# Optimization experiments

Hardware: AMD Instinct MI355X
Metric: run time of the kernel (lower is better)

The kernel has to match this reference:

```python
import jax, jax.numpy as jnp
import numpy as np

B, N, CIN, H, D, K = 8, 1000, 16, 64, 16, 3  # batch, nodes, in_dim, hidden, embed_dim, cheb_k
XIN = CIN + H  # GRU concat input dim


def setup_inputs() -> dict:
    key = jax.random.key(0)
    ks = jax.random.split(key, 18)
    f = lambda k, s, sc=1.0: jax.random.normal(k, s, dtype=jnp.float32) * sc
    inp = {}
    inp['x1'] = f(ks[0], (B, N, CIN)); inp['x2'] = f(ks[1], (B, N, CIN)); inp['x3'] = f(ks[2], (B, N, CIN))
    inp['state1'] = f(ks[3], (B, N, H)); inp['state2'] = f(ks[4], (B, N, H)); inp['state3'] = f(ks[5], (B, N, H))
    for i, name in enumerate(['support1', 'support2', 'support3']):
        a = jax.random.uniform(ks[6 + i], (N, N), dtype=jnp.float32)
        inp[name] = a / a.sum(-1, keepdims=True)  # row-stochastic graph, keeps Chebyshev stable
    inp['embeddings1'] = f(ks[9], (N, D), 0.1); inp['embeddings2'] = f(ks[10], (N, D), 0.1); inp['embeddings3'] = f(ks[11], (N, D), 0.1)
    inp['mode_embedding'] = f(ks[12], (3, D), 0.5)
    # xavier-normal-ish scales for the hypernet weight pools
    inp['Wg'] = f(ks[13], (D, K * XIN, 2 * H), (2.0 / (K * XIN * 2 * H + D * 2 * H)) ** 0.5)
    inp['Bg'] = f(ks[14], (D, 2 * H), (2.0 / (D + 2 * H)) ** 0.5)
    inp['Wu'] = f(ks[15], (D, K * XIN, H), (2.0 / (K * XIN * H + D * H)) ** 0.5)
    inp['Bu'] = f(ks[16], (D, H), (2.0 / (D + H)) ** 0.5)
    return inp


def _cheb_gcn(x, support, emb, wp, bp):
    # x:[B,N,C], support:[N,N], emb:[N,D], wp:[D,K*C,O], bp:[D,O]
    # Chebyshev recurrence applied directly to features (equivalent to building T_k(support))
    terms = [x, jnp.einsum('nm,bmc->bnc', support, x)]
    for _ in range(2, K):
        terms.append(2.0 * jnp.einsum('nm,bmc->bnc', support, terms[-1]) - terms[-2])
    x_g = jnp.concatenate(terms, axis=-1)  # [B,N,K*C]
    # meta_axis='S': per-node weights = emb @ wp ; fused contraction
    out = jnp.einsum('bni,nd,dio->bno', x_g, emb, wp) + emb @ bp  # [B,N,O]
    return out


def _cell(x, state, support, emb, me, Wg, Bg, Wu, Bu):
    # me:[D] mode embedding scales the shared pools (einsum 'mc,cdf->mcdf' -> pick mode m)
    zr = jax.nn.sigmoid(_cheb_gcn(jnp.concatenate([x, state], -1), support, emb,
                                  me[:, None, None] * Wg, me[:, None] * Bg))
    z, r = jnp.split(zr, 2, axis=-1)
    hc = jnp.tanh(_cheb_gcn(jnp.concatenate([x, z * state], -1), support, emb,
                            me[:, None, None] * Wu, me[:, None] * Bu))
    return r * state + (1.0 - r) * hc


def reference(x1, x2, x3, state1, state2, state3, support1, support2, support3,
              embeddings1, embeddings2, embeddings3, mode_embedding, Wg, Bg, Wu, Bu):
    h1 = _cell(x1, state1, support1, embeddings1, mode_embedding[0], Wg, Bg, Wu, Bu)
    h2 = _cell(x2, state2, support2, embeddings2, mode_embedding[1], Wg, Bg, Wu, Bu)
    h3 = _cell(x3, state3, support3, embeddings3, mode_embedding[2], Wg, Bg, Wu, Bu)
    return (h1, h2, h3)
```

## Files before the change

### kernel.cpp

```cpp
#include <hip/hip_runtime.h>
#include <math.h>


typedef __attribute__((ext_vector_type(8))) short s16x8;
typedef __attribute__((ext_vector_type(4))) float f32x4;
typedef unsigned short u16;
typedef unsigned int u32;
typedef unsigned long long u64;

__device__ __forceinline__ u32 f2bf(float f) {
  union { float f; u32 u; } v; v.f = f;
  return (v.u + 0x7FFFu + ((v.u >> 16) & 1u)) >> 16;
}
__device__ __forceinline__ float bf2f(u16 h) {
  union { u32 u; float f; } v; v.u = (u32)h << 16; return v.f;
}
__device__ __forceinline__ void glds16(const u16* g, u16* l) {
  __builtin_amdgcn_global_load_lds(
      (const __attribute__((address_space(1))) void*)g,
      (__attribute__((address_space(3))) void*)l, 16, 0, 0);
}

#define E0 3145728
#define E1 1966080
#define E2 1920000
#define E3 384000
#define E4 384000
#define E5 384000
#define E6 119808

struct PrepArgs {
  const float* x[3]; const float* st[3]; const float* S[3];
  u16 *S16, *Xt, *Ag, *AgU, *T1t, *ZSt, *SZ1t;
};

__global__ void prep(PrepArgs P) {
  long idx = (long)blockIdx.x * 256 + threadIdx.x;
  if (idx < E0) {
    int m = (int)(idx >> 20); int rem = (int)(idx & 1048575);
    int n = rem >> 10, k = rem & 1023;
    float v = (n < 1000 && k < 1000) ? P.S[m][n * 1000 + k] : 0.f;
    P.S16[(size_t)m * 1048576 + rem] = (u16)f2bf(v); return;
  }
  idx -= E0;
  if (idx < E1) {
    int m = (int)(idx / 655360); int rem = (int)(idx % 655360);
    int col = rem >> 10, nn = rem & 1023;
    int b = col / 80, c = col % 80;
    float v = 0.f;
    if (nn < 1000) v = (c < 16) ? P.x[m][(b * 1000 + nn) * 16 + c]
                                : P.st[m][(b * 1000 + nn) * 64 + c - 16];
    P.Xt[(size_t)m * 655360 + rem] = (u16)f2bf(v); return;
  }
  idx -= E1;
  if (idx < E2) {
    int m = (int)(idx / 640000); int rem = (int)(idx % 640000);
    int r = rem / 80, c = rem % 80;
    int n = r >> 3, b = r & 7;
    float v = (c < 16) ? P.x[m][(b * 1000 + n) * 16 + c]
                       : P.st[m][(b * 1000 + n) * 64 + c - 16];
    P.Ag[(size_t)m * 2048000 + (size_t)r * 256 + c] = (u16)f2bf(v); return;
  }
  idx -= E2;
  if (idx < E3) {
    int m = (int)(idx / 128000); int rem = (int)(idx % 128000);
    int r = rem / 16, c = 240 + rem % 16;
    P.Ag[(size_t)m * 2048000 + (size_t)r * 256 + c] = 0; return;
  }
  idx -= E3;
  if (idx < E4) {
    int m = (int)(idx / 128000); int rem = (int)(idx % 128000);
    int r = rem / 16, c = rem % 16;
    int n = r >> 3, b = r & 7;
    P.AgU[(size_t)m * 2048000 + (size_t)r * 256 + c] =
        (u16)f2bf(P.x[m][(b * 1000 + n) * 16 + c]); return;
  }
  idx -= E4;
  if (idx < E5) {
    int m = (int)(idx / 128000); int rem = (int)(idx % 128000);
    int r = rem / 16, c = 240 + rem % 16;
    P.AgU[(size_t)m * 2048000 + (size_t)r * 256 + c] = 0; return;
  }
  idx -= E5;
  if (idx < E6) {
    int m = (int)(idx / 39936); int rem = (int)(idx % 39936);
    if (rem < 15360) { int col = rem / 24, j = rem % 24;
      P.T1t[(size_t)m * 655360 + col * 1024 + 1000 + j] = 0; }
    else if (rem < 27648) { int e = rem - 15360; int col = e / 24, j = e % 24;
      P.ZSt[(size_t)m * 524288 + col * 1024 + 1000 + j] = 0; }
    else { int e = rem - 27648; int col = e / 24, j = e % 24;
      P.SZ1t[(size_t)m * 524288 + col * 1024 + 1000 + j] = 0; }
    return;
  }
}

__global__ void bias_kernel(const float* __restrict__ e0, const float* __restrict__ e1,
                            const float* __restrict__ e2, const float* __restrict__ me,
                            const float* __restrict__ Bp, int O, float* __restrict__ outB) {
  int idx = blockIdx.x * blockDim.x + threadIdx.x;
  int total = 3 * 1000 * O;
  if (idx >= total) return;
  int mode = idx / (1000 * O);
  int rem  = idx % (1000 * O);
  int n = rem / O, o = rem % O;
  const float* emb = (mode == 0) ? e0 : (mode == 1) ? e1 : e2;
  float s = 0.f;
#pragma unroll
  for (int d = 0; d < 16; ++d)
    s += emb[n * 16 + d] * me[mode * 16 + d] * Bp[d * O + o];
  outB[idx] = s;
}

__global__ void packW_kernel(const float* __restrict__ Wg, const float* __restrict__ Wu,
                             u16* __restrict__ BtG, u16* __restrict__ BtU) {
  int idx = blockIdx.x * blockDim.x + threadIdx.x;
  if (idx >= (2048 + 1024) * 256) return;
  if (idx < 2048 * 256) {
    int col = idx >> 8, k = idx & 255;
    int d = col >> 7, o = col & 127;
    BtG[idx] = (k < 240) ? (u16)f2bf(Wg[d * 30720 + k * 128 + o]) : (u16)0;
  } else {
    int i2 = idx - 2048 * 256;
    int col = i2 >> 8, k = i2 & 255;
    int d = col >> 6, o = col & 63;
    BtU[i2] = (k < 240) ? (u16)f2bf(Wu[d * 15360 + k * 64 + o]) : (u16)0;
  }
}

struct ChebArgs2 {
  const u16* S16[3]; const u16* A[3]; const u16* Res[3];
  u16* Yt[3]; u16* AgA[3]; u16* AgX[3];
};

__global__ __launch_bounds__(256, 2) void cheb_v4(ChebArgs2 g, int fdiv, int agbase,
                                                  float alpha, float beta, int flags) {
  const int mode = blockIdx.z;
  const u16* __restrict__ Ab = g.A[mode];
  const u16* __restrict__ Sb = g.S16[mode];

  __shared__ u16 As[64 * 64];
  __shared__ u16 Bs[64 * 64];

  const int t = threadIdx.x;
  const int row0 = blockIdx.y * 64, n0 = blockIdx.x * 64;
  const int lane = t & 63, wid = t >> 6;
  const int l16 = lane & 15, quad = lane >> 4;
  const int wy = (wid >> 1) * 32, wx = (wid & 1) * 32;

  f32x4 acc[2][2];
#pragma unroll
  for (int a = 0; a < 2; ++a)
#pragma unroll
    for (int b = 0; b < 2; ++b) acc[a][b] = (f32x4){0.f, 0.f, 0.f, 0.f};

  for (int k0 = 0; k0 < 1024; k0 += 64) {
#pragma unroll
    for (int p = 0; p < 2; ++p) {
      int idx = p * 256 + t; int row = idx >> 3; int cs = (idx & 7) ^ (row & 7);
      glds16(Ab + (size_t)(row0 + row) * 1024 + k0 + cs * 8, &As[idx * 8]);
    }
#pragma unroll
    for (int p = 0; p < 2; ++p) {
      int idx = p * 256 + t; int row = idx >> 3; int cs = (idx & 7) ^ (row & 7);
      glds16(Sb + (size_t)(n0 + row) * 1024 + k0 + cs * 8, &Bs[idx * 8]);
    }
    __syncthreads();
    s16x8 af[2][2], bf[2][2];
#pragma unroll
    for (int mi = 0; mi < 2; ++mi) {
      int row = wy + mi * 16 + l16;
#pragma unroll
      for (int ks = 0; ks < 2; ++ks) {
        int cl = (ks * 4 + quad) ^ (row & 7);
        af[mi][ks] = *(const s16x8*)&As[row * 64 + cl * 8];
      }
    }
#pragma unroll
    for (int ni = 0; ni < 2; ++ni) {
      int row = wx + ni * 16 + l16;
#pragma unroll
      for (int ks = 0; ks < 2; ++ks) {
        int cl = (ks * 4 + quad) ^ (row & 7);
        bf[ni][ks] = *(const s16x8*)&Bs[row * 64 + cl * 8];
      }
    }
#pragma unroll
    for (int ks = 0; ks < 2; ++ks)
#pragma unroll
      for (int mi = 0; mi < 2; ++mi)
#pragma unroll
        for (int ni = 0; ni < 2; ++ni)
          acc[mi][ni] = __builtin_amdgcn_mfma_f32_16x16x32_bf16(af[mi][ks], bf[ni][ks], acc[mi][ni], 0, 0, 0);
    __syncthreads();
  }

#pragma unroll
  for (int mi = 0; mi < 2; ++mi) {
    int frow0 = row0 + wy + mi * 16 + quad * 4;
    int b = frow0 / fdiv, c0 = frow0 - b * fdiv;
#pragma unroll
    for (int ni = 0; ni < 2; ++ni) {
      int n = n0 + wx + ni * 16 + l16;
      if (n < 1000) {
        u16 pk[4];
#pragma unroll
        for (int r = 0; r < 4; ++r) {
          float v = alpha * acc[mi][ni][r];
          if (flags & 1) v += beta * bf2f(g.Res[mode][(size_t)(frow0 + r) * 1024 + n]);
          u16 h = (u16)f2bf(v);
          pk[r] = h;
          if (flags & 2) g.Yt[mode][(size_t)(frow0 + r) * 1024 + n] = h;
        }
        u64 pv = (u64)pk[0] | ((u64)pk[1] << 16) | ((u64)pk[2] << 32) | ((u64)pk[3] << 48);
        *(u64*)&g.AgA[mode][(size_t)(n * 8 + b) * 256 + agbase + c0] = pv;
        if ((flags & 4) && c0 < 16)
          *(u64*)&g.AgX[mode][(size_t)(n * 8 + b) * 256 + agbase + c0] = pv;
      }
    }
  }
}

struct Meta3Args {
  const u16* Ag;
  const u16* Bt;
  const float* emb[3];
  const float* me;
  const float* Bias;
  const float* state[3];
  u16* ZSt;
  u16* AgU;
  float* Rb;
  float* out;
};

__global__ __launch_bounds__(256, 2) void meta3(Meta3Args A, int is_gate, int O) {
  const int mode = blockIdx.z;
  const int row0 = blockIdx.y * 64;
  const int n0 = row0 >> 3;

  __shared__ u16 As[64 * 256];
  __shared__ u16 Bs[64 * 256];
  __shared__ float ewS[8][17];

  const int t = threadIdx.x;
  if (t < 128) {
    int nl = t >> 4, d = t & 15;
    ewS[nl][d] = A.emb[mode][(n0 + nl) * 16 + d] * A.me[mode * 16 + d];
  }

  const int lane = t & 63, wid = t >> 6;
  const int l16 = lane & 15, quad = lane >> 4;
  const int wy = (wid >> 1) * 32, wx = (wid & 1) * 32;
  const u16* Agm = A.Ag + (size_t)mode * 2048000;

#pragma unroll
  for (int p = 0; p < 8; ++p) {
    int idx = p * 256 + t; int row = idx >> 5; int cs = (idx & 31) ^ (row & 7);
    glds16(Agm + (size_t)(row0 + row) * 256 + cs * 8, &As[idx * 8]);
  }
  __syncthreads();

  s16x8 afr[2][8];
#pragma unroll
  for (int mi = 0; mi < 2; ++mi) {
    int row = wy + mi * 16 + l16;
#pragma unroll
    for (int ki = 0; ki < 8; ++ki) {
      int cl = (ki * 4 + quad) ^ (row & 7);
      afr[mi][ki] = *(const s16x8*)&As[row * 256 + cl * 8];
    }
  }

  f32x4 outacc[2][2][2];
#pragma unroll
  for (int a = 0; a < 2; ++a)
#pragma unroll
    for (int b = 0; b < 2; ++b)
#pragma unroll
      for (int c = 0; c < 2; ++c) outacc[a][b][c] = (f32x4){0.f, 0.f, 0.f, 0.f};

  const int shift = (O == 128) ? 1 : 0;
  const int ntiles = O >> 2;

  for (int tl = 0; tl < ntiles; ++tl) {
    const int d = tl >> shift;
    const int oc = tl & shift;
    __syncthreads();
    const int brow0 = d * O + oc * 64;
#pragma unroll
    for (int p = 0; p < 8; ++p) {
      int idx = p * 256 + t; int row = idx >> 5; int cs = (idx & 31) ^ (row & 7);
      glds16(A.Bt + (size_t)(brow0 + row) * 256 + cs * 8, &Bs[idx * 8]);
    }
    __syncthreads();

    f32x4 acc[2][2];
#pragma unroll
    for (int a = 0; a < 2; ++a)
#pragma unroll
      for (int b = 0; b < 2; ++b) acc[a][b] = (f32x4){0.f, 0.f, 0.f, 0.f};

#pragma unroll
    for (int ki = 0; ki < 8; ++ki) {
      s16x8 bfr[2];
#pragma unroll
      for (int ni = 0; ni < 2; ++ni) {
        int row = wx + ni * 16 + l16;
        int cl = (ki * 4 + quad) ^ (row & 7);
        bfr[ni] = *(const s16x8*)&Bs[row * 256 + cl * 8];
      }
#pragma unroll
      for (int mi = 0; mi < 2; ++mi)
#pragma unroll
        for (int ni = 0; ni < 2; ++ni)
          acc[mi][ni] = __builtin_amdgcn_mfma_f32_16x16x32_bf16(afr[mi][ki], bfr[ni], acc[mi][ni], 0, 0, 0);
    }

#pragma unroll
    for (int mi = 0; mi < 2; ++mi) {
      int nl = (wy + mi * 16 + quad * 4) >> 3;
      float s = ewS[nl][d];
#pragma unroll
      for (int ni = 0; ni < 2; ++ni)
#pragma unroll
        for (int r = 0; r < 4; ++r)
          outacc[oc][mi][ni][r] += s * acc[mi][ni][r];
    }
  }

#pragma unroll
  for (int oc = 0; oc <= shift; ++oc)
#pragma unroll
    for (int mi = 0; mi < 2; ++mi)
#pragma unroll
      for (int ni = 0; ni < 2; ++ni)
#pragma unroll
        for (int r = 0; r < 4; ++r) {
          int row = row0 + wy + mi * 16 + quad * 4 + r;
          int n = row >> 3, b = row & 7;
          int o = oc * 64 + wx + ni * 16 + l16;
          float pre = outacc[oc][mi][ni][r] + A.Bias[(size_t)mode * 1000 * O + n * O + o];
          if (is_gate) {
            float sg = 1.f / (1.f + __expf(-pre));
            if (o < 64) {
              float st = A.state[mode][(b * 1000 + n) * 64 + o];
              float zs = sg * st;
              A.ZSt[(size_t)mode * 524288 + (size_t)(b * 64 + o) * 1024 + n] = (u16)f2bf(zs);
              A.AgU[(size_t)mode * 2048000 + (size_t)row * 256 + 16 + o] = (u16)f2bf(zs);
            } else {
              A.Rb[(size_t)mode * 512000 + row * 64 + (o - 64)] = sg;
            }
          } else {
            float hc = tanhf(pre);
            float rr = A.Rb[(size_t)mode * 512000 + row * 64 + o];
            float st = A.state[mode][(b * 1000 + n) * 64 + o];
            A.out[(size_t)mode * 512000 + (b * 1000 + n) * 64 + o] = rr * st + (1.f - rr) * hc;
          }
        }
}

extern "C" void kernel_launch(void* const* d_in, const int* in_sizes, int n_in,
                              void* d_out, int out_size, void* d_ws, size_t ws_size,
                              hipStream_t stream) {
  const float* x[3]   = {(const float*)d_in[0], (const float*)d_in[1], (const float*)d_in[2]};
  const float* st[3]  = {(const float*)d_in[3], (const float*)d_in[4], (const float*)d_in[5]};
  const float* S[3]   = {(const float*)d_in[6], (const float*)d_in[7], (const float*)d_in[8]};
  const float* emb[3] = {(const float*)d_in[9], (const float*)d_in[10], (const float*)d_in[11]};
  const float* me = (const float*)d_in[12];
  const float* Wg = (const float*)d_in[13];
  const float* Bg = (const float*)d_in[14];
  const float* Wu = (const float*)d_in[15];
  const float* Bu = (const float*)d_in[16];
  float* out = (float*)d_out;

  float* BiG = (float*)d_ws;
  float* BiU = BiG + 384000;
  float* Rb  = BiU + 192000;
  u16* S16 = (u16*)(Rb + 1536000);
  u16* Xt  = S16 + 3145728;
  u16* T1t = Xt + 1966080;
  u16* ZSt = T1t + 1966080;
  u16* SZ1t= ZSt + 1572864;
  u16* Ag  = SZ1t + 1572864;
  u16* AgU = Ag + 6144000;
  u16* BtG = AgU + 6144000;
  u16* BtU = BtG + 524288;

  {
    PrepArgs P;
    for (int m = 0; m < 3; ++m) { P.x[m] = x[m]; P.st[m] = st[m]; P.S[m] = S[m]; }
    P.S16 = S16; P.Xt = Xt; P.Ag = Ag; P.AgU = AgU; P.T1t = T1t; P.ZSt = ZSt; P.SZ1t = SZ1t;
    prep<<<32436, 256, 0, stream>>>(P);
  }
  bias_kernel<<<1500, 256, 0, stream>>>(emb[0], emb[1], emb[2], me, Bg, 128, BiG);
  bias_kernel<<<750, 256, 0, stream>>>(emb[0], emb[1], emb[2], me, Bu, 64, BiU);
  packW_kernel<<<3072, 256, 0, stream>>>(Wg, Wu, BtG, BtU);

  {
    ChebArgs2 a;
    for (int m = 0; m < 3; ++m) {
      a.S16[m] = S16 + (size_t)m * 1048576; a.A[m] = Xt + (size_t)m * 655360;
      a.Res[m] = nullptr; a.Yt[m] = T1t + (size_t)m * 655360;
      a.AgA[m] = Ag + (size_t)m * 2048000; a.AgX[m] = AgU + (size_t)m * 2048000;
    }
    cheb_v4<<<dim3(16, 10, 3), 256, 0, stream>>>(a, 80, 80, 1.f, 0.f, 2 | 4);
  }
  {
    ChebArgs2 a;
    for (int m = 0; m < 3; ++m) {
      a.S16[m] = S16 + (size_t)m * 1048576; a.A[m] = T1t + (size_t)m * 655360;
      a.Res[m] = Xt + (size_t)m * 655360; a.Yt[m] = nullptr;
      a.AgA[m] = Ag + (size_t)m * 2048000; a.AgX[m] = AgU + (size_t)m * 2048000;
    }
    cheb_v4<<<dim3(16, 10, 3), 256, 0, stream>>>(a, 80, 160, 2.f, -1.f, 1 | 4);
  }
  {
    Meta3Args a;
    a.Ag = Ag; a.Bt = BtG; a.me = me; a.Bias = BiG;
    a.ZSt = ZSt; a.AgU = AgU; a.Rb = Rb; a.out = out;
    for (int m = 0; m < 3; ++m) { a.emb[m] = emb[m]; a.state[m] = st[m]; }
    meta3<<<dim3(1, 125, 3), 256, 0, stream>>>(a, 1, 128);
  }
  {
    ChebArgs2 a;
    for (int m = 0; m < 3; ++m) {
      a.S16[m] = S16 + (size_t)m * 1048576; a.A[m] = ZSt + (size_t)m * 524288;
      a.Res[m] = nullptr; a.Yt[m] = SZ1t + (size_t)m * 524288;
      a.AgA[m] = AgU + (size_t)m * 2048000; a.AgX[m] = nullptr;
    }
    cheb_v4<<<dim3(16, 8, 3), 256, 0, stream>>>(a, 64, 96, 1.f, 0.f, 2);
  }
  {
    ChebArgs2 a;
    for (int m = 0; m < 3; ++m) {
      a.S16[m] = S16 + (size_t)m * 1048576; a.A[m] = SZ1t + (size_t)m * 524288;
      a.Res[m] = ZSt + (size_t)m * 524288; a.Yt[m] = nullptr;
      a.AgA[m] = AgU + (size_t)m * 2048000; a.AgX[m] = nullptr;
    }
    cheb_v4<<<dim3(16, 8, 3), 256, 0, stream>>>(a, 64, 176, 2.f, -1.f, 1);
  }
  {
    Meta3Args a;
    a.Ag = AgU; a.Bt = BtU; a.me = me; a.Bias = BiU;
    a.ZSt = ZSt; a.AgU = AgU; a.Rb = Rb; a.out = out;
    for (int m = 0; m < 3; ++m) { a.emb[m] = emb[m]; a.state[m] = st[m]; }
    meta3<<<dim3(1, 125, 3), 256, 0, stream>>>(a, 0, 64);
  }
}
```

Baseline: 270.4 us.

## Read B operands directly from global memory in cheb and meta kernels

New measurement: 432.0 us. +59.7%, slower.

```diff
diff --git a/kernel.cpp b/kernel.cpp
--- a/kernel.cpp
+++ b/kernel.cpp
@@ -132,66 +132,59 @@
   u16* Yt[3]; u16* AgA[3]; u16* AgX[3];
 };
 
-__global__ __launch_bounds__(256, 2) void cheb_v4(ChebArgs2 g, int fdiv, int agbase,
+__global__ __launch_bounds__(256, 2) void cheb_v5(ChebArgs2 g, int fdiv, int agbase,
                                                   float alpha, float beta, int flags) {
   const int mode = blockIdx.z;
   const u16* __restrict__ Ab = g.A[mode];
   const u16* __restrict__ Sb = g.S16[mode];
 
-  __shared__ u16 As[64 * 64];
-  __shared__ u16 Bs[64 * 64];
+  __shared__ u16 As[64 * 256];
 
   const int t = threadIdx.x;
-  const int row0 = blockIdx.y * 64, n0 = blockIdx.x * 64;
+  const int row0 = blockIdx.y * 64, n0 = blockIdx.x * 128;
   const int lane = t & 63, wid = t >> 6;
   const int l16 = lane & 15, quad = lane >> 4;
-  const int wy = (wid >> 1) * 32, wx = (wid & 1) * 32;
-
-  f32x4 acc[2][2];
+  const int wy = (wid >> 1) * 32, wx = (wid & 1) * 64;
+
+  f32x4 acc[2][4];
 #pragma unroll
   for (int a = 0; a < 2; ++a)
 #pragma unroll
-    for (int b = 0; b < 2; ++b) acc[a][b] = (f32x4){0.f, 0.f, 0.f, 0.f};
-
-  for (int k0 = 0; k0 < 1024; k0 += 64) {
-#pragma unroll
-    for (int p = 0; p < 2; ++p) {
-      int idx = p * 256 + t; int row = idx >> 3; int cs = (idx & 7) ^ (row & 7);
+    for (int b = 0; b < 4; ++b) acc[a][b] = (f32x4){0.f, 0.f, 0.f, 0.f};
+
+  const u16* Bbase = Sb + (size_t)(n0 + wx + l16) * 1024 + quad * 8;
+
+  for (int k0 = 0; k0 < 1024; k0 += 256) {
+#pragma unroll
+    for (int p = 0; p < 8; ++p) {
+      int idx = p * 256 + t; int row = idx >> 5; int cs = (idx & 31) ^ (row & 7);
       glds16(Ab + (size_t)(row0 + row) * 1024 + k0 + cs * 8, &As[idx * 8]);
     }
-#pragma unroll
-    for (int p = 0; p < 2; ++p) {
-      int idx = p * 256 + t; int row = idx >> 3; int cs = (idx & 7) ^ (row & 7);
-      glds16(Sb + (size_t)(n0 + row) * 1024 + k0 + cs * 8, &Bs[idx * 8]);
-    }
     __syncthreads();
-    s16x8 af[2][2], bf[2][2];
+    s16x8 afr[2][8];
 #pragma unroll
     for (int mi = 0; mi < 2; ++mi) {
       int row = wy + mi * 16 + l16;
 #pragma unroll
-      for (int ks = 0; ks < 2; ++ks) {
-        int cl = (ks * 4 + quad) ^ (row & 7);
-        af[mi][ks] = *(const s16x8*)&As[row * 64 + cl * 8];
+      for (int ki = 0; ki < 8; ++ki) {
+        int cl = (ki * 4 + quad) ^ (row & 7);
+        afr[mi][ki] = *(const s16x8*)&As[row * 256 + cl * 8];
       }
     }
-#pragma unroll
-    for (int ni = 0; ni < 2; ++ni) {
-      int row = wx + ni * 16 + l16;
-#pragma unroll
-      for (int ks = 0; ks < 2; ++ks) {
-        int cl = (ks * 4 + quad) ^ (row & 7);
-        bf[ni][ks] = *(const s16x8*)&Bs[row * 64 + cl * 8];
-      }
-    }
-#pragma unroll
-    for (int ks = 0; ks < 2; ++ks)
+    __syncthreads();
+
+#pragma unroll
+    for (int ki = 0; ki < 8; ++ki) {
+      s16x8 bfr[4];
+#pragma unroll
+      for (int ni = 0; ni < 4; ++ni)
+        bfr[ni] = *(const s16x8*)(Bbase + (size_t)ni * 16 * 1024 + k0 + ki * 32);
 #pragma unroll
       for (int mi = 0; mi < 2; ++mi)
 #pragma unroll
-        for (int ni = 0; ni < 2; ++ni)
-          acc[mi][ni] = __builtin_amdgcn_mfma_f32_16x16x32_bf16(af[mi][ks], bf[ni][ks], acc[mi][ni], 0, 0, 0);
-    __syncthreads();
+        for (int ni = 0; ni < 4; ++ni)
+          acc[mi][ni] = __builtin_amdgcn_mfma_f32_16x16x32_bf16(afr[mi][ki], bfr[ni], acc[mi][ni], 0, 0, 0);
+    }
   }
 
 #pragma unroll
@@ -199,7 +192,7 @@
     int frow0 = row0 + wy + mi * 16 + quad * 4;
     int b = frow0 / fdiv, c0 = frow0 - b * fdiv;
 #pragma unroll
-    for (int ni = 0; ni < 2; ++ni) {
+    for (int ni = 0; ni < 4; ++ni) {
       int n = n0 + wx + ni * 16 + l16;
       if (n < 1000) {
         u16 pk[4];
@@ -233,13 +226,12 @@
   float* out;
 };
 
-__global__ __launch_bounds__(256, 2) void meta3(Meta3Args A, int is_gate, int O) {
+__global__ __launch_bounds__(256, 2) void meta4(Meta3Args A, int is_gate, int O) {
   const int mode = blockIdx.z;
   const int row0 = blockIdx.y * 64;
   const int n0 = row0 >> 3;
 
   __shared__ u16 As[64 * 256];
-  __shared__ u16 Bs[64 * 256];
   __shared__ float ewS[8][17];
 
   const int t = threadIdx.x;
@@ -282,17 +274,12 @@
   const int shift = (O == 128) ? 1 : 0;
   const int ntiles = O >> 2;
 
+  const u16* Bb = A.Bt + (size_t)(wx + l16) * 256 + quad * 8;
+
   for (int tl = 0; tl < ntiles; ++tl) {
     const int d = tl >> shift;
     const int oc = tl & shift;
-    __syncthreads();
-    const int brow0 = d * O + oc * 64;
-#pragma unroll
-    for (int p = 0; p < 8; ++p) {
-      int idx = p * 256 + t; int row = idx >> 5; int cs = (idx & 31) ^ (row & 7);
-      glds16(A.Bt + (size_t)(brow0 + row) * 256 + cs * 8, &Bs[idx * 8]);
-    }
-    __syncthreads();
+    const u16* Bt0 = Bb + (size_t)(d * O + oc * 64) * 256;
 
     f32x4 acc[2][2];
 #pragma unroll
@@ -304,11 +291,8 @@
     for (int ki = 0; ki < 8; ++ki) {
       s16x8 bfr[2];
 #pragma unroll
-      for (int ni = 0; ni < 2; ++ni) {
-        int row = wx + ni * 16 + l16;
-        int cl = (ki * 4 + quad) ^ (row & 7);
-        bfr[ni] = *(const s16x8*)&Bs[row * 256 + cl * 8];
-      }
+      for (int ni = 0; ni < 2; ++ni)
+        bfr[ni] = *(const s16x8*)(Bt0 + (size_t)ni * 16 * 256 + ki * 32);
 #pragma unroll
       for (int mi = 0; mi < 2; ++mi)
 #pragma unroll
@@ -403,7 +387,7 @@
       a.Res[m] = nullptr; a.Yt[m] = T1t + (size_t)m * 655360;
       a.AgA[m] = Ag + (size_t)m * 2048000; a.AgX[m] = AgU + (size_t)m * 2048000;
     }
-    cheb_v4<<<dim3(16, 10, 3), 256, 0, stream>>>(a, 80, 80, 1.f, 0.f, 2 | 4);
+    cheb_v5<<<dim3(8, 10, 3), 256, 0, stream>>>(a, 80, 80, 1.f, 0.f, 2 | 4);
   }
   {
     ChebArgs2 a;
@@ -412,14 +396,14 @@
       a.Res[m] = Xt + (size_t)m * 655360; a.Yt[m] = nullptr;
       a.AgA[m] = Ag + (size_t)m * 2048000; a.AgX[m] = AgU + (size_t)m * 2048000;
     }
-    cheb_v4<<<dim3(16, 10, 3), 256, 0, stream>>>(a, 80, 160, 2.f, -1.f, 1 | 4);
+    cheb_v5<<<dim3(8, 10, 3), 256, 0, stream>>>(a, 80, 160, 2.f, -1.f, 1 | 4);
   }
   {
     Meta3Args a;
     a.Ag = Ag; a.Bt = BtG; a.me = me; a.Bias = BiG;
     a.ZSt = ZSt; a.AgU = AgU; a.Rb = Rb; a.out = out;
     for (int m = 0; m < 3; ++m) { a.emb[m] = emb[m]; a.state[m] = st[m]; }
-    meta3<<<dim3(1, 125, 3), 256, 0, stream>>>(a, 1, 128);
+    meta4<<<dim3(1, 125, 3), 256, 0, stream>>>(a, 1, 128);
   }
   {
     ChebArgs2 a;
@@ -428,7 +412,7 @@
       a.Res[m] = nullptr; a.Yt[m] = SZ1t + (size_t)m * 524288;
       a.AgA[m] = AgU + (size_t)m * 2048000; a.AgX[m] = nullptr;
     }
-    cheb_v4<<<dim3(16, 8, 3), 256, 0, stream>>>(a, 64, 96, 1.f, 0.f, 2);
+    cheb_v5<<<dim3(8, 8, 3), 256, 0, stream>>>(a, 64, 96, 1.f, 0.f, 2);
   }
   {
     ChebArgs2 a;
@@ -437,13 +421,13 @@
       a.Res[m] = ZSt + (size_t)m * 524288; a.Yt[m] = nullptr;
       a.AgA[m] = AgU + (size_t)m * 2048000; a.AgX[m] = nullptr;
     }
-    cheb_v4<<<dim3(16, 8, 3), 256, 0, stream>>>(a, 64, 176, 2.f, -1.f, 1);
+    cheb_v5<<<dim3(8, 8, 3), 256, 0, stream>>>(a, 64, 176, 2.f, -1.f, 1);
   }
   {
     Meta3Args a;
     a.Ag = AgU; a.Bt = BtU; a.me = me; a.Bias = BiU;
     a.ZSt = ZSt; a.AgU = AgU; a.Rb = Rb; a.out = out;
     for (int m = 0; m < 3; ++m) { a.emb[m] = emb[m]; a.state[m] = st[m]; }
-    meta3<<<dim3(1, 125, 3), 256, 0, stream>>>(a, 0, 64);
-  }
-}
+    meta4<<<dim3(1, 125, 3), 256, 0, stream>>>(a, 0, 64);
+  }
+}
```

## Double-buffer LDS staging in Chebyshev and hypernet GEMM kernels

Applied to the files above, without the earlier changes.

After: 286.6 us. 1.06x slower.

```diff
diff --git a/kernel.cpp b/kernel.cpp
--- a/kernel.cpp
+++ b/kernel.cpp
@@ -132,14 +132,14 @@
   u16* Yt[3]; u16* AgA[3]; u16* AgX[3];
 };
 
-__global__ __launch_bounds__(256, 2) void cheb_v4(ChebArgs2 g, int fdiv, int agbase,
+__global__ __launch_bounds__(256, 4) void cheb_v6(ChebArgs2 g, int fdiv, int agbase,
                                                   float alpha, float beta, int flags) {
   const int mode = blockIdx.z;
   const u16* __restrict__ Ab = g.A[mode];
   const u16* __restrict__ Sb = g.S16[mode];
 
-  __shared__ u16 As[64 * 64];
-  __shared__ u16 Bs[64 * 64];
+  __shared__ u16 As[2][64 * 64];
+  __shared__ u16 Bs[2][64 * 64];
 
   const int t = threadIdx.x;
   const int row0 = blockIdx.y * 64, n0 = blockIdx.x * 64;
@@ -147,24 +147,33 @@
   const int l16 = lane & 15, quad = lane >> 4;
   const int wy = (wid >> 1) * 32, wx = (wid & 1) * 32;
 
+#define STAGE_CHEB(kk, bb)                                                      \
+  {                                                                             \
+    _Pragma("unroll")                                                           \
+    for (int p = 0; p < 2; ++p) {                                               \
+      int idx = p * 256 + t; int row = idx >> 3; int cs = (idx & 7) ^ (row & 7);\
+      glds16(Ab + (size_t)(row0 + row) * 1024 + (kk) + cs * 8, &As[bb][idx * 8]);\
+    }                                                                           \
+    _Pragma("unroll")                                                           \
+    for (int p = 0; p < 2; ++p) {                                               \
+      int idx = p * 256 + t; int row = idx >> 3; int cs = (idx & 7) ^ (row & 7);\
+      glds16(Sb + (size_t)(n0 + row) * 1024 + (kk) + cs * 8, &Bs[bb][idx * 8]); \
+    }                                                                           \
+  }
+
   f32x4 acc[2][2];
 #pragma unroll
   for (int a = 0; a < 2; ++a)
 #pragma unroll
     for (int b = 0; b < 2; ++b) acc[a][b] = (f32x4){0.f, 0.f, 0.f, 0.f};
 
-  for (int k0 = 0; k0 < 1024; k0 += 64) {
-#pragma unroll
-    for (int p = 0; p < 2; ++p) {
-      int idx = p * 256 + t; int row = idx >> 3; int cs = (idx & 7) ^ (row & 7);
-      glds16(Ab + (size_t)(row0 + row) * 1024 + k0 + cs * 8, &As[idx * 8]);
-    }
-#pragma unroll
-    for (int p = 0; p < 2; ++p) {
-      int idx = p * 256 + t; int row = idx >> 3; int cs = (idx & 7) ^ (row & 7);
-      glds16(Sb + (size_t)(n0 + row) * 1024 + k0 + cs * 8, &Bs[idx * 8]);
-    }
+  STAGE_CHEB(0, 0);
+
+  for (int it = 0; it < 16; ++it) {
     __syncthreads();
+    if (it < 15) STAGE_CHEB((it + 1) * 64, (it + 1) & 1);
+    const u16* Ac = As[it & 1];
+    const u16* Bc = Bs[it & 1];
     s16x8 af[2][2], bf[2][2];
 #pragma unroll
     for (int mi = 0; mi < 2; ++mi) {
@@ -172,7 +181,7 @@
 #pragma unroll
       for (int ks = 0; ks < 2; ++ks) {
         int cl = (ks * 4 + quad) ^ (row & 7);
-        af[mi][ks] = *(const s16x8*)&As[row * 64 + cl * 8];
+        af[mi][ks] = *(const s16x8*)&Ac[row * 64 + cl * 8];
       }
     }
 #pragma unroll
@@ -181,7 +190,7 @@
 #pragma unroll
       for (int ks = 0; ks < 2; ++ks) {
         int cl = (ks * 4 + quad) ^ (row & 7);
-        bf[ni][ks] = *(const s16x8*)&Bs[row * 64 + cl * 8];
+        bf[ni][ks] = *(const s16x8*)&Bc[row * 64 + cl * 8];
       }
     }
 #pragma unroll
@@ -191,7 +200,6 @@
 #pragma unroll
         for (int ni = 0; ni < 2; ++ni)
           acc[mi][ni] = __builtin_amdgcn_mfma_f32_16x16x32_bf16(af[mi][ks], bf[ni][ks], acc[mi][ni], 0, 0, 0);
-    __syncthreads();
   }
 
 #pragma unroll
@@ -233,13 +241,12 @@
   float* out;
 };
 
-__global__ __launch_bounds__(256, 2) void meta3(Meta3Args A, int is_gate, int O) {
+__global__ __launch_bounds__(256, 2) void meta5(Meta3Args A, int is_gate, int O) {
   const int mode = blockIdx.z;
   const int row0 = blockIdx.y * 64;
   const int n0 = row0 >> 3;
 
-  __shared__ u16 As[64 * 256];
-  __shared__ u16 Bs[64 * 256];
+  __shared__ u16 Bs[2][64 * 256];
   __shared__ float ewS[8][17];
 
   const int t = threadIdx.x;
@@ -253,46 +260,45 @@
   const int wy = (wid >> 1) * 32, wx = (wid & 1) * 32;
   const u16* Agm = A.Ag + (size_t)mode * 2048000;
 
-#pragma unroll
-  for (int p = 0; p < 8; ++p) {
-    int idx = p * 256 + t; int row = idx >> 5; int cs = (idx & 31) ^ (row & 7);
-    glds16(Agm + (size_t)(row0 + row) * 256 + cs * 8, &As[idx * 8]);
-  }
-  __syncthreads();
-
-  s16x8 afr[2][8];
-#pragma unroll
-  for (int mi = 0; mi < 2; ++mi) {
-    int row = wy + mi * 16 + l16;
-#pragma unroll
-    for (int ki = 0; ki < 8; ++ki) {
-      int cl = (ki * 4 + quad) ^ (row & 7);
-      afr[mi][ki] = *(const s16x8*)&As[row * 256 + cl * 8];
-    }
-  }
-
-  f32x4 outacc[2][2][2];
-#pragma unroll
-  for (int a = 0; a < 2; ++a)
-#pragma unroll
-    for (int b = 0; b < 2; ++b)
-#pragma unroll
-      for (int c = 0; c < 2; ++c) outacc[a][b][c] = (f32x4){0.f, 0.f, 0.f, 0.f};
+#define STAGE_B(brow0, bb)                                                      \
+  {                                                                             \
+    _Pragma("unroll")                                                           \
+    for (int p = 0; p < 8; ++p) {                                               \
+      int idx = p * 256 + t; int row = idx >> 5; int cs = (idx & 31) ^ (row & 7);\
+      glds16(A.Bt + (size_t)((brow0) + row) * 256 + cs * 8, &Bs[bb][idx * 8]);  \
+    }                                                                           \
+  }
 
   const int shift = (O == 128) ? 1 : 0;
   const int ntiles = O >> 2;
 
+  STAGE_B(0, 0);
+
+  s16x8 afr[2][8];
+#pragma unroll
+  for (int mi = 0; mi < 2; ++mi) {
+    const u16* arow = Agm + (size_t)(row0 + wy + mi * 16 + l16) * 256 + quad * 8;
+#pragma unroll
+    for (int ki = 0; ki < 8; ++ki)
+      afr[mi][ki] = *(const s16x8*)(arow + ki * 32);
+  }
+
+  f32x4 outacc[2][2][2];
+#pragma unroll
+  for (int a = 0; a < 2; ++a)
+#pragma unroll
+    for (int b = 0; b < 2; ++b)
+#pragma unroll
+      for (int c = 0; c < 2; ++c) outacc[a][b][c] = (f32x4){0.f, 0.f, 0.f, 0.f};
+
   for (int tl = 0; tl < ntiles; ++tl) {
-    const int d = tl >> shift;
-    const int oc = tl & shift;
     __syncthreads();
-    const int brow0 = d * O + oc * 64;
-#pragma unroll
-    for (int p = 0; p < 8; ++p) {
-      int idx = p * 256 + t; int row = idx >> 5; int cs = (idx & 31) ^ (row & 7);
-      glds16(A.Bt + (size_t)(brow0 + row) * 256 + cs * 8, &Bs[idx * 8]);
-    }
-    __syncthreads();
+    if (tl + 1 < ntiles) {
+      int dn = (tl + 1) >> shift, ocn = (tl + 1) & shift;
+      STAGE_B(dn * O + ocn * 64, (tl + 1) & 1);
+    }
+    const u16* Bc = Bs[tl & 1];
+    const int d = tl >> shift, oc = tl & shift;
 
     f32x4 acc[2][2];
 #pragma unroll
@@ -307,7 +313,7 @@
       for (int ni = 0; ni < 2; ++ni) {
         int row = wx + ni * 16 + l16;
         int cl = (ki * 4 + quad) ^ (row & 7);
-        bfr[ni] = *(const s16x8*)&Bs[row * 256 + cl * 8];
+        bfr[ni] = *(const s16x8*)&Bc[row * 256 + cl * 8];
       }
 #pragma unroll
       for (int mi = 0; mi < 2; ++mi)
@@ -403,7 +409,7 @@
       a.Res[m] = nullptr; a.Yt[m] = T1t + (size_t)m * 655360;
       a.AgA[m] = Ag + (size_t)m * 2048000; a.AgX[m] = AgU + (size_t)m * 2048000;
     }
-    cheb_v4<<<dim3(16, 10, 3), 256, 0, stream>>>(a, 80, 80, 1.f, 0.f, 2 | 4);
+    cheb_v6<<<dim3(16, 10, 3), 256, 0, stream>>>(a, 80, 80, 1.f, 0.f, 2 | 4);
   }
   {
     ChebArgs2 a;
@@ -412,14 +418,14 @@
       a.Res[m] = Xt + (size_t)m * 655360; a.Yt[m] = nullptr;
       a.AgA[m] = Ag + (size_t)m * 2048000; a.AgX[m] = AgU + (size_t)m * 2048000;
     }
-    cheb_v4<<<dim3(16, 10, 3), 256, 0, stream>>>(a, 80, 160, 2.f, -1.f, 1 | 4);
+    cheb_v6<<<dim3(16, 10, 3), 256, 0, stream>>>(a, 80, 160, 2.f, -1.f, 1 | 4);
   }
   {
     Meta3Args a;
     a.Ag = Ag; a.Bt = BtG; a.me = me; a.Bias = BiG;
     a.ZSt = ZSt; a.AgU = AgU; a.Rb = Rb; a.out = out;
     for (int m = 0; m < 3; ++m) { a.emb[m] = emb[m]; a.state[m] = st[m]; }
-    meta3<<<dim3(1, 125, 3), 256, 0, stream>>>(a, 1, 128);
+    meta5<<<dim3(1, 125, 3), 256, 0, stream>>>(a, 1, 128);
   }
   {
     ChebArgs2 a;
@@ -428,7 +434,7 @@
       a.Res[m] = nullptr; a.Yt[m] = SZ1t + (size_t)m * 524288;
       a.AgA[m] = AgU + (size_t)m * 2048000; a.AgX[m] = nullptr;
     }
-    cheb_v4<<<dim3(16, 8, 3), 256, 0, stream>>>(a, 64, 96, 1.f, 0.f, 2);
+    cheb_v6<<<dim3(16, 8, 3), 256, 0, stream>>>(a, 64, 96, 1.f, 0.f, 2);
   }
   {
     ChebArgs2 a;
@@ -437,13 +443,13 @@
       a.Res[m] = ZSt + (size_t)m * 524288; a.Yt[m] = nullptr;
       a.AgA[m] = AgU + (size_t)m * 2048000; a.AgX[m] = nullptr;
     }
-    cheb_v4<<<dim3(16, 8, 3), 256, 0, stream>>>(a, 64, 176, 2.f, -1.f, 1);
+    cheb_v6<<<dim3(16, 8, 3), 256, 0, stream>>>(a, 64, 176, 2.f, -1.f, 1);
   }
   {
     Meta3Args a;
     a.Ag = AgU; a.Bt = BtU; a.me = me; a.Bias = BiU;
     a.ZSt = ZSt; a.AgU = AgU; a.Rb = Rb; a.out = out;
     for (int m = 0; m < 3; ++m) { a.emb[m] = emb[m]; a.state[m] = st[m]; }
-    meta3<<<dim3(1, 125, 3), 256, 0, stream>>>(a, 0, 64);
-  }
-}
+    meta5<<<dim3(1, 125, 3), 256, 0, stream>>>(a, 0, 64);
+  }
+}
```
